# Performance work log

Measured on AMD Instinct MI355X. Metric: run time of the kernel, lower is better.

The kernel has to match this reference:

```python
import jax, jax.numpy as jnp
import numpy as np

GROUPS = 32
EPS = 1e-6


def group_norm(x, scale, bias):
    B, C, H, W = x.shape
    xg = x.reshape(B, GROUPS, C // GROUPS, H, W)
    mean = xg.mean(axis=(2, 3, 4), keepdims=True)
    var = xg.var(axis=(2, 3, 4), keepdims=True)
    xg = (xg - mean) * jax.lax.rsqrt(var + EPS)
    x = xg.reshape(B, C, H, W)
    return x * scale[None, :, None, None] + bias[None, :, None, None]


def conv1x1(x, w, b):
    # x: [B,C,H,W], w: [O,C], b: [O]
    return jnp.einsum('bchw,oc->bohw', x, w) + b[None, :, None, None]


def setup_inputs() -> dict:
    key = jax.random.key(0)
    ks = jax.random.split(key, 6)
    B, C, H, W = 8, 256, 64, 64
    s = 1.0 / np.sqrt(C)
    return {
        'x': jax.random.normal(ks[0], (B, C, H, W), dtype=jnp.float32),
        'gn_scale': jnp.ones((C,), dtype=jnp.float32),
        'gn_bias': jnp.zeros((C,), dtype=jnp.float32),
        'wq': jax.random.normal(ks[1], (C, C), dtype=jnp.float32) * s,
        'bq': jnp.zeros((C,), dtype=jnp.float32),
        'wk': jax.random.normal(ks[2], (C, C), dtype=jnp.float32) * s,
        'bk': jnp.zeros((C,), dtype=jnp.float32),
        'wv': jax.random.normal(ks[3], (C, C), dtype=jnp.float32) * s,
        'bv': jnp.zeros((C,), dtype=jnp.float32),
        'wo': jax.random.normal(ks[4], (C, C), dtype=jnp.float32) * s,
        'bo': jnp.zeros((C,), dtype=jnp.float32),
    }


def reference(x, gn_scale, gn_bias, wq, bq, wk, bk, wv, bv, wo, bo):
    skip = x
    h = group_norm(x, gn_scale, gn_bias)
    B, C, H, W = h.shape
    N = H * W
    q = conv1x1(h, wq, bq).reshape(B, C, N)  # [B,C,N]
    k = conv1x1(h, wk, bk).reshape(B, C, N)
    v = conv1x1(h, wv, bv).reshape(B, C, N)
    # scores[b,i,j] = sum_c q[b,c,i] k[b,c,j] / sqrt(C)
    scores = jnp.einsum('bci,bcj->bij', q, k) / jnp.sqrt(jnp.float32(C))
    a = jax.nn.softmax(scores, axis=2)  # softmax over keys j
    # z[b,c,i] = sum_j v[b,c,j] a[b,i,j]
    z = jnp.einsum('bcj,bij->bci', v, a).reshape(B, C, H, W)
    z = conv1x1(z, wo, bo)
    return skip + z
```

## Files before the change

kernel.cpp:

```cpp
#include <hip/hip_runtime.h>
#include <math.h>

typedef __bf16 bf16;
typedef __bf16 bf16x8 __attribute__((ext_vector_type(8)));
typedef __bf16 bf16x4 __attribute__((ext_vector_type(4)));
typedef float  f32x4  __attribute__((ext_vector_type(4)));
typedef float  f32x16 __attribute__((ext_vector_type(16)));
typedef unsigned int u32;
typedef unsigned char u8;
typedef u32 u32x2 __attribute__((ext_vector_type(2)));
typedef u32 u32x4 __attribute__((ext_vector_type(4)));
typedef int  i32x8 __attribute__((ext_vector_type(8)));

#define MFMA(a, b, c)   __builtin_amdgcn_mfma_f32_16x16x32_bf16((a), (b), (c), 0, 0, 0)
#define MFMAS(a, b, c)                                                           \
  __builtin_amdgcn_mfma_scale_f32_32x32x64_f8f6f4((a), (b), (c), 0, 0,           \
                                                  0, 0x7f7f7f7f, 0, 0x7f7f7f7f)

#define GLOAD_LDS16(g, l)                                                        \
  __builtin_amdgcn_global_load_lds(                                              \
      (const __attribute__((address_space(1))) void*)(g),                        \
      (__attribute__((address_space(3))) void*)(l), 16, 0, 0)

static constexpr int B_ = 8, C_ = 256, N_ = 4096;
static constexpr float QSCALE = 0.09016844005556021f;
static constexpr float PBIAS  = 2.0f;

static constexpr size_t HT_OFF = 0;
static constexpr size_t QT_OFF = 16777216;
static constexpr size_t KT_OFF = 25165824;
static constexpr size_t V_OFF  = 33554432;
static constexpr size_t WQ_OFF = 41943040;
static constexpr size_t WK_OFF = WQ_OFF + 131072;
static constexpr size_t WV_OFF = WK_OFF + 131072;
static constexpr size_t WO_OFF = WV_OFF + 131072;
static constexpr size_t ZN_OFF = WO_OFF + 131072;
static constexpr size_t LS_OFF = ZN_OFF + 33554432;
static constexpr size_t PART_ELEMS = (size_t)B_ * C_ * N_;

__global__ __launch_bounds__(256) void wconv_kernel(
    const float* __restrict__ wq, const float* __restrict__ wk,
    const float* __restrict__ wv, const float* __restrict__ wo,
    bf16* __restrict__ oq, bf16* __restrict__ ok, bf16* __restrict__ ov, bf16* __restrict__ oo) {
  int i = blockIdx.x * 256 + threadIdx.x;
  oq[i] = (bf16)wq[i];
  ok[i] = (bf16)wk[i];
  ov[i] = (bf16)wv[i];
  oo[i] = (bf16)wo[i];
}

__global__ __launch_bounds__(512) void gn_kernel(
    const float* __restrict__ x, const float* __restrict__ gsc, const float* __restrict__ gbi,
    bf16* __restrict__ hT) {
  int b = blockIdx.x >> 5, g = blockIdx.x & 31, c0 = g * 8;
  int t = threadIdx.x;
  const float* base = x + ((size_t)(b * C_ + c0)) * N_;
  __shared__ bf16 xl[32768];
  float s = 0.f, ss = 0.f;
  const f32x4* b4 = (const f32x4*)base;
#pragma unroll
  for (int p = 0; p < 16; p++) {
    int u = t + p * 512;
    f32x4 v = b4[u];
    s  += v[0] + v[1] + v[2] + v[3];
    ss += v[0] * v[0] + v[1] * v[1] + v[2] * v[2] + v[3] * v[3];
    bf16x4 xv;
#pragma unroll
    for (int e = 0; e < 4; e++) xv[e] = (bf16)v[e];
    *(bf16x4*)(xl + u * 4) = xv;
  }
#pragma unroll
  for (int off = 1; off < 64; off <<= 1) {
    s  += __shfl_xor(s, off);
    ss += __shfl_xor(ss, off);
  }
  __shared__ float red[16];
  if ((t & 63) == 0) { red[(t >> 6) * 2] = s; red[(t >> 6) * 2 + 1] = ss; }
  __syncthreads();
  s = 0.f; ss = 0.f;
#pragma unroll
  for (int r = 0; r < 8; r++) { s += red[r * 2]; ss += red[r * 2 + 1]; }
  float mean = s * (1.f / 32768.f);
  float var  = ss * (1.f / 32768.f) - mean * mean;
  float rstd = rsqrtf(var + 1e-6f);
  float aa[8], bb[8];
#pragma unroll
  for (int cc = 0; cc < 8; cc++) {
    aa[cc] = rstd * gsc[c0 + cc];
    bb[cc] = gbi[c0 + cc] - mean * aa[cc];
  }
#pragma unroll
  for (int ii = 0; ii < 8; ii++) {
    int i = t + ii * 512;
    bf16x8 o;
#pragma unroll
    for (int cc = 0; cc < 8; cc++) o[cc] = (bf16)((float)xl[cc * 4096 + i] * aa[cc] + bb[cc]);
    *(bf16x8*)(hT + ((size_t)(b * N_ + i)) * C_ + c0) = o;
  }
}

__global__ __launch_bounds__(256) void qkv_kernel(
    const bf16* __restrict__ hT,
    const bf16* __restrict__ wqb, const bf16* __restrict__ wkb, const bf16* __restrict__ wvb,
    const float* __restrict__ bq, const float* __restrict__ bk, const float* __restrict__ bv,
    u8* __restrict__ qT8, u8* __restrict__ kT8, u8* __restrict__ v8) {
  int b = blockIdx.x >> 6, i0 = (blockIdx.x & 63) << 6;
  int t = threadIdx.x, w = t >> 6, lane = t & 63, quad = lane >> 4, l15 = lane & 15;
  __shared__ bf16 hl[64 * 264];
#pragma unroll
  for (int p = 0; p < 8; p++) {
    int u = t + p * 256, r = u >> 5, c16 = u & 31;
    *(bf16x8*)(hl + r * 264 + c16 * 8) =
        *(const bf16x8*)(hT + ((size_t)(b * N_ + i0 + r)) * C_ + c16 * 8);
  }
  __syncthreads();
  int cw0 = w * 64;

  f32x4 aq[4][4], ak[4][4];
#pragma unroll
  for (int a = 0; a < 4; a++)
#pragma unroll
    for (int bb2 = 0; bb2 < 4; bb2++) { aq[a][bb2] = (f32x4){0.f,0.f,0.f,0.f}; ak[a][bb2] = (f32x4){0.f,0.f,0.f,0.f}; }
  for (int kc = 0; kc < 8; kc++) {
    bf16x8 hb[4];
#pragma unroll
    for (int it = 0; it < 4; it++)
      hb[it] = *(const bf16x8*)(hl + (it * 16 + l15) * 264 + kc * 32 + quad * 8);
#pragma unroll
    for (int ct = 0; ct < 4; ct++) {
      bf16x8 wqf = *(const bf16x8*)(wqb + ((size_t)(cw0 + ct * 16 + l15)) * C_ + kc * 32 + quad * 8);
      bf16x8 wkf = *(const bf16x8*)(wkb + ((size_t)(cw0 + ct * 16 + l15)) * C_ + kc * 32 + quad * 8);
#pragma unroll
      for (int it = 0; it < 4; it++) {
        aq[ct][it] = MFMA(wqf, hb[it], aq[ct][it]);
        ak[ct][it] = MFMA(wkf, hb[it], ak[ct][it]);
      }
    }
  }
#pragma unroll
  for (int ct = 0; ct < 4; ct++)
#pragma unroll
    for (int it = 0; it < 4; it++) {
      int c4 = cw0 + ct * 16 + quad * 4;
      int i  = i0 + it * 16 + l15;
      f32x4 bq4 = *(const f32x4*)(bq + c4);
      f32x4 bk4 = *(const f32x4*)(bk + c4);
      float qv[4], kv[4];
#pragma unroll
      for (int r = 0; r < 4; r++) {
        qv[r] = (aq[ct][it][r] + bq4[r]) * (QSCALE * 4.0f);
        kv[r] = (ak[ct][it][r] + bk4[r]) * 0.25f;
      }
      u32 qd = (u32)__builtin_amdgcn_cvt_pk_fp8_f32(qv[0], qv[1], 0, false);
      qd = (u32)__builtin_amdgcn_cvt_pk_fp8_f32(qv[2], qv[3], (int)qd, true);
      u32 kd = (u32)__builtin_amdgcn_cvt_pk_fp8_f32(kv[0], kv[1], 0, false);
      kd = (u32)__builtin_amdgcn_cvt_pk_fp8_f32(kv[2], kv[3], (int)kd, true);
      *(u32*)(qT8 + ((size_t)(b * N_ + i)) * C_ + c4) = qd;
      *(u32*)(kT8 + ((size_t)(b * N_ + i)) * C_ + c4) = kd;
    }

  f32x4 av[4][4];
#pragma unroll
  for (int a = 0; a < 4; a++)
#pragma unroll
    for (int bb2 = 0; bb2 < 4; bb2++) av[a][bb2] = (f32x4){0.f,0.f,0.f,0.f};
  for (int kc = 0; kc < 8; kc++) {
    bf16x8 ha[4];
#pragma unroll
    for (int it = 0; it < 4; it++)
      ha[it] = *(const bf16x8*)(hl + (it * 16 + l15) * 264 + kc * 32 + quad * 8);
#pragma unroll
    for (int ct = 0; ct < 4; ct++) {
      bf16x8 wvf = *(const bf16x8*)(wvb + ((size_t)(cw0 + ct * 16 + l15)) * C_ + kc * 32 + quad * 8);
#pragma unroll
      for (int it = 0; it < 4; it++) av[it][ct] = MFMA(ha[it], wvf, av[it][ct]);
    }
  }
#pragma unroll
  for (int it = 0; it < 4; it++)
#pragma unroll
    for (int ct = 0; ct < 4; ct++) {
      int c  = cw0 + ct * 16 + l15;
      int i4 = i0 + it * 16 + quad * 4;
      float bvc = bv[c];
      float vv4[4];
#pragma unroll
      for (int r = 0; r < 4; r++) vv4[r] = av[it][ct][r] + bvc;
      u32 vd = (u32)__builtin_amdgcn_cvt_pk_fp8_f32(vv4[0], vv4[1], 0, false);
      vd = (u32)__builtin_amdgcn_cvt_pk_fp8_f32(vv4[2], vv4[3], (int)vd, true);
      *(u32*)(v8 + ((size_t)(b * C_ + c)) * N_ + i4) = vd;
    }
}

__global__ __launch_bounds__(256, 2) void attn_kernel(
    const u8* __restrict__ qT8, const u8* __restrict__ kT8, const u8* __restrict__ v8,
    bf16* __restrict__ zNum, float* __restrict__ lsum) {
  int blk = blockIdx.x;
  int sp = blk >> 8;
  int b = blk & 7;
  int i0 = ((blk >> 3) & 31) << 7;
  int t = threadIdx.x, w = t >> 6, lane = t & 63;
  int r31 = lane & 31, h = lane >> 5;
  __shared__ __align__(16) u8 lds8[2 * 32768];

  int iw = i0 + w * 32;
  const u8* qrow = qT8 + ((size_t)(b * N_ + iw + r31)) * C_ + h * 32;
  i32x8 qB[4];
#pragma unroll
  for (int m = 0; m < 4; m++) qB[m] = *(const i32x8*)(qrow + m * 64);

  f32x16 of[8];
#pragma unroll
  for (int ct = 0; ct < 8; ct++)
#pragma unroll
    for (int e = 0; e < 16; e++) of[ct][e] = 0.f;
  float lacc = 0.f;

  int ks = r31 & 7;
  int kr_off = lane >> 4;
  int kc_pos = lane & 15;
  int vr_off = lane >> 2;
  int vc_pos = lane & 3;

  auto stage = [&](int jts, int buf) {
    int j0s = sp * 2048 + jts * 64;
    u8* kb = lds8 + buf * 32768;
    u8* vb = kb + 16384;
#pragma unroll
    for (int p = 0; p < 4; p++) {
      int idx = w * 4 + p;
      int r = idx * 4 + kr_off;
      int chunk = kc_pos ^ (r & 7);
      GLOAD_LDS16(kT8 + ((size_t)(b * N_ + j0s + r)) * C_ + chunk * 16, kb + idx * 1024);
    }
#pragma unroll
    for (int p = 0; p < 4; p++) {
      int idx = w * 4 + p;
      int c = idx * 16 + vr_off;
      int chunk = vc_pos ^ ((c >> 1) & 3);
      GLOAD_LDS16(v8 + ((size_t)(b * C_ + c)) * N_ + j0s + chunk * 16, vb + idx * 1024);
    }
  };

  stage(0, 0);

  for (int jt = 0; jt < 32; jt++) {
    int cur = jt & 1;
    __builtin_amdgcn_s_barrier();
    stage(jt < 31 ? jt + 1 : 31, cur ^ 1);
    asm volatile("s_waitcnt vmcnt(8)" ::: "memory");
    __builtin_amdgcn_s_barrier();
    const u8* kTl = lds8 + cur * 32768;
    const u8* vl  = kTl + 16384;

    u32 PG0[4], PG1[4];
#pragma unroll
    for (int g = 0; g < 2; g++) {
      f32x16 st;
#pragma unroll
      for (int e = 0; e < 16; e++) st[e] = -PBIAS;
      const u8* krow = kTl + (g * 32 + r31) * 256;
#pragma unroll
      for (int m = 0; m < 4; m++) {
        int cd = m * 4 + h * 2;
        union { i32x8 v; u32x4 h4[2]; } kf;
        kf.h4[0] = *(const u32x4*)(krow + ((cd ^ ks) * 16));
        kf.h4[1] = *(const u32x4*)(krow + (((cd + 1) ^ ks) * 16));
        st = MFMAS(kf.v, qB[m], st);
      }
#pragma unroll
      for (int b4 = 0; b4 < 4; b4++) {
        float p0 = __builtin_amdgcn_exp2f(st[b4 * 4 + 0]);
        float p1 = __builtin_amdgcn_exp2f(st[b4 * 4 + 1]);
        float p2 = __builtin_amdgcn_exp2f(st[b4 * 4 + 2]);
        float p3 = __builtin_amdgcn_exp2f(st[b4 * 4 + 3]);
        lacc += (p0 + p1) + (p2 + p3);
        u32 d = (u32)__builtin_amdgcn_cvt_pk_fp8_f32(p0, p1, 0, false);
        d = (u32)__builtin_amdgcn_cvt_pk_fp8_f32(p2, p3, (int)d, true);
        if (g == 0) PG0[b4] = d; else PG1[b4] = d;
      }
    }

    u32 A[8];
#pragma unroll
    for (int b4 = 0; b4 < 4; b4++) {
      u32x2 rr = __builtin_amdgcn_permlane32_swap(PG0[b4], PG1[b4], false, false);
      A[2 * b4]     = rr[0];
      A[2 * b4 + 1] = rr[1];
    }
    i32x8 pA;
#pragma unroll
    for (int e = 0; e < 8; e++) pA[e] = (int)A[e];

#pragma unroll
    for (int ct = 0; ct < 8; ct++) {
      int c = ct * 32 + r31;
      int vs = (c >> 1) & 3;
      const u8* vrow = vl + c * 64;
      union { i32x8 v; u32x4 h4[2]; } vB;
      vB.h4[0] = *(const u32x4*)(vrow + (((2 * h) ^ vs) * 16));
      vB.h4[1] = *(const u32x4*)(vrow + (((2 * h + 1) ^ vs) * 16));
      of[ct] = MFMAS(pA, vB.v, of[ct]);
    }
  }

  lacc += __shfl_xor(lacc, 32);
  if (h == 0)
    lsum[((size_t)(sp * 8 + b)) * N_ + iw + r31] = lacc;
  bf16* zn = zNum + (size_t)sp * PART_ELEMS;
#pragma unroll
  for (int ct = 0; ct < 8; ct++) {
    int c = ct * 32 + r31;
#pragma unroll
    for (int g = 0; g < 4; g++) {
      bf16x4 zv;
#pragma unroll
      for (int e = 0; e < 4; e++) zv[e] = (bf16)of[ct][g * 4 + e];
      int i4 = iw + 8 * g + 4 * h;
      *(bf16x4*)(zn + ((size_t)(b * C_ + c)) * N_ + i4) = zv;
    }
  }
}

__global__ __launch_bounds__(256) void combine_kernel(
    const bf16* __restrict__ zNum, const float* __restrict__ lsum,
    const bf16* __restrict__ wob, const float* __restrict__ bo,
    const float* __restrict__ x, float* __restrict__ out) {
  int b = blockIdx.x >> 6, i0 = (blockIdx.x & 63) << 6;
  int t = threadIdx.x, w = t >> 6, lane = t & 63, quad = lane >> 4, l15 = lane & 15;
  __shared__ bf16 zl[64 * 264];
  __shared__ float linv[64];

  if (t < 64) {
    size_t ii = (size_t)b * N_ + i0 + t;
    linv[t] = 1.f / (lsum[ii] + lsum[ii + (size_t)8 * N_]);
  }
  __syncthreads();

#pragma unroll
  for (int p = 0; p < 16; p++) {
    int u = t + p * 256, c = u >> 4, ii = (u & 15) * 4;
    size_t base = ((size_t)(b * C_ + c)) * N_ + i0 + ii;
    bf16x4 z0 = *(const bf16x4*)(zNum + base);
    bf16x4 z1 = *(const bf16x4*)(zNum + PART_ELEMS + base);
#pragma unroll
    for (int e = 0; e < 4; e++)
      zl[(ii + e) * 264 + c] = (bf16)(((float)z0[e] + (float)z1[e]) * linv[ii + e]);
  }
  __syncthreads();

  f32x4 oa[4][4];
#pragma unroll
  for (int a = 0; a < 4; a++)
#pragma unroll
    for (int bb2 = 0; bb2 < 4; bb2++) oa[a][bb2] = (f32x4){0.f, 0.f, 0.f, 0.f};
  for (int kc = 0; kc < 8; kc++) {
    bf16x8 za[4];
#pragma unroll
    for (int it = 0; it < 4; it++)
      za[it] = *(const bf16x8*)(zl + (it * 16 + l15) * 264 + kc * 32 + quad * 8);
#pragma unroll
    for (int ctl = 0; ctl < 4; ctl++) {
      bf16x8 wf = *(const bf16x8*)(wob + ((size_t)(w * 64 + ctl * 16 + l15)) * C_ + kc * 32 + quad * 8);
#pragma unroll
      for (int it = 0; it < 4; it++) oa[ctl][it] = MFMA(za[it], wf, oa[ctl][it]);
    }
  }
#pragma unroll
  for (int ctl = 0; ctl < 4; ctl++)
#pragma unroll
    for (int it = 0; it < 4; it++) {
      int c = w * 64 + ctl * 16 + l15;
      size_t base = ((size_t)(b * C_ + c)) * N_ + i0 + it * 16 + quad * 4;
      f32x4 xs = *(const f32x4*)(x + base);
      float boc = bo[c];
      f32x4 o4;
#pragma unroll
      for (int r = 0; r < 4; r++) o4[r] = oa[ctl][it][r] + boc + xs[r];
      *(f32x4*)(out + base) = o4;
    }
}

extern "C" void kernel_launch(void* const* d_in, const int* in_sizes, int n_in,
                              void* d_out, int out_size, void* d_ws, size_t ws_size,
                              hipStream_t stream) {
  const float* x   = (const float*)d_in[0];
  const float* gsc = (const float*)d_in[1];
  const float* gbi = (const float*)d_in[2];
  const float* wq  = (const float*)d_in[3];
  const float* bq  = (const float*)d_in[4];
  const float* wk  = (const float*)d_in[5];
  const float* bk  = (const float*)d_in[6];
  const float* wv  = (const float*)d_in[7];
  const float* bv  = (const float*)d_in[8];
  const float* wo  = (const float*)d_in[9];
  const float* bo  = (const float*)d_in[10];

  char* ws = (char*)d_ws;
  bf16* hT   = (bf16*)(ws + HT_OFF);
  u8*   qT8  = (u8*)(ws + QT_OFF);
  u8*   kT8  = (u8*)(ws + KT_OFF);
  u8*   v8   = (u8*)(ws + V_OFF);
  bf16* wqb  = (bf16*)(ws + WQ_OFF);
  bf16* wkb  = (bf16*)(ws + WK_OFF);
  bf16* wvb  = (bf16*)(ws + WV_OFF);
  bf16* wob  = (bf16*)(ws + WO_OFF);
  bf16* zNum = (bf16*)(ws + ZN_OFF);
  float* lsum = (float*)(ws + LS_OFF);

  wconv_kernel<<<256, 256, 0, stream>>>(wq, wk, wv, wo, wqb, wkb, wvb, wob);
  gn_kernel<<<256, 512, 0, stream>>>(x, gsc, gbi, hT);
  qkv_kernel<<<512, 256, 0, stream>>>(hT, wqb, wkb, wvb, bq, bk, bv, qT8, kT8, v8);
  attn_kernel<<<512, 256, 0, stream>>>(qT8, kT8, v8, zNum, lsum);
  combine_kernel<<<512, 256, 0, stream>>>(zNum, lsum, wob, bo, x, (float*)d_out);
}
```

Before: 251.8 us.

## Split attention keys four ways, shrink LDS to three buffers for higher occupancy

Templates the attention kernel on the number of key splits and launches 4 splits (1024 blocks) when the workspace is large enough, so more blocks are available to fill the CUs. LDS is cut from two K+V double buffers to two K buffers plus one V buffer, with an extra wait and barrier before the PV step, and launch bounds are raised to 3 blocks per CU. The hT region is reused for the first partial-output buffer, and the combine kernel sums SP partials. The cost is more partial-output traffic in the combine kernel and an extra barrier per key tile.

```diff
diff --git a/kernel.cpp b/kernel.cpp
--- a/kernel.cpp
+++ b/kernel.cpp
@@ -34,9 +34,12 @@
 static constexpr size_t WK_OFF = WQ_OFF + 131072;
 static constexpr size_t WV_OFF = WK_OFF + 131072;
 static constexpr size_t WO_OFF = WV_OFF + 131072;
-static constexpr size_t ZN_OFF = WO_OFF + 131072;
-static constexpr size_t LS_OFF = ZN_OFF + 33554432;
+static constexpr size_t LS_OFF = WO_OFF + 131072;
+static constexpr size_t ZN2_OFF = LS_OFF + 524288;
 static constexpr size_t PART_ELEMS = (size_t)B_ * C_ * N_;
+static constexpr size_t PART_BYTES = PART_ELEMS * 2;
+static constexpr size_t WS_NEED4 = ZN2_OFF + 3 * PART_BYTES;
+static constexpr size_t WS_NEED2 = ZN2_OFF + 1 * PART_BYTES;
 
 __global__ __launch_bounds__(256) void wconv_kernel(
     const float* __restrict__ wq, const float* __restrict__ wk,
@@ -192,16 +195,19 @@
     }
 }
 
-__global__ __launch_bounds__(256, 2) void attn_kernel(
+template <int SP>
+__global__ __launch_bounds__(256, 3) void attn_kernel(
     const u8* __restrict__ qT8, const u8* __restrict__ kT8, const u8* __restrict__ v8,
-    bf16* __restrict__ zNum, float* __restrict__ lsum) {
+    bf16* __restrict__ zn0, bf16* __restrict__ znR, float* __restrict__ lsum) {
+  constexpr int NKEY = N_ / SP;
+  constexpr int NJT  = NKEY / 64;
   int blk = blockIdx.x;
   int sp = blk >> 8;
   int b = blk & 7;
   int i0 = ((blk >> 3) & 31) << 7;
   int t = threadIdx.x, w = t >> 6, lane = t & 63;
   int r31 = lane & 31, h = lane >> 5;
-  __shared__ __align__(16) u8 lds8[2 * 32768];
+  __shared__ __align__(16) u8 lds8[3 * 16384];
 
   int iw = i0 + w * 32;
   const u8* qrow = qT8 + ((size_t)(b * N_ + iw + r31)) * C_ + h * 32;
@@ -221,11 +227,11 @@
   int kc_pos = lane & 15;
   int vr_off = lane >> 2;
   int vc_pos = lane & 3;
-
-  auto stage = [&](int jts, int buf) {
-    int j0s = sp * 2048 + jts * 64;
-    u8* kb = lds8 + buf * 32768;
-    u8* vb = kb + 16384;
+  int spBase = sp * NKEY;
+  u8* vb = lds8 + 32768;
+
+  auto stageK = [&](int jts, u8* kb) {
+    int j0s = spBase + jts * 64;
 #pragma unroll
     for (int p = 0; p < 4; p++) {
       int idx = w * 4 + p;
@@ -233,6 +239,9 @@
       int chunk = kc_pos ^ (r & 7);
       GLOAD_LDS16(kT8 + ((size_t)(b * N_ + j0s + r)) * C_ + chunk * 16, kb + idx * 1024);
     }
+  };
+  auto stageV = [&](int jts) {
+    int j0s = spBase + jts * 64;
 #pragma unroll
     for (int p = 0; p < 4; p++) {
       int idx = w * 4 + p;
@@ -242,16 +251,15 @@
     }
   };
 
-  stage(0, 0);
-
-  for (int jt = 0; jt < 32; jt++) {
-    int cur = jt & 1;
+  stageK(0, lds8);
+
+  for (int jt = 0; jt < NJT; jt++) {
     __builtin_amdgcn_s_barrier();
-    stage(jt < 31 ? jt + 1 : 31, cur ^ 1);
+    stageV(jt);
+    stageK(jt < NJT - 1 ? jt + 1 : jt, lds8 + (((jt + 1) & 1) << 14));
     asm volatile("s_waitcnt vmcnt(8)" ::: "memory");
     __builtin_amdgcn_s_barrier();
-    const u8* kTl = lds8 + cur * 32768;
-    const u8* vl  = kTl + 16384;
+    const u8* kTl = lds8 + ((jt & 1) << 14);
 
     u32 PG0[4], PG1[4];
 #pragma unroll
@@ -292,11 +300,14 @@
 #pragma unroll
     for (int e = 0; e < 8; e++) pA[e] = (int)A[e];
 
+    asm volatile("s_waitcnt vmcnt(4)" ::: "memory");
+    __builtin_amdgcn_s_barrier();
+
 #pragma unroll
     for (int ct = 0; ct < 8; ct++) {
       int c = ct * 32 + r31;
       int vs = (c >> 1) & 3;
-      const u8* vrow = vl + c * 64;
+      const u8* vrow = vb + c * 64;
       union { i32x8 v; u32x4 h4[2]; } vB;
       vB.h4[0] = *(const u32x4*)(vrow + (((2 * h) ^ vs) * 16));
       vB.h4[1] = *(const u32x4*)(vrow + (((2 * h + 1) ^ vs) * 16));
@@ -307,7 +318,7 @@
   lacc += __shfl_xor(lacc, 32);
   if (h == 0)
     lsum[((size_t)(sp * 8 + b)) * N_ + iw + r31] = lacc;
-  bf16* zn = zNum + (size_t)sp * PART_ELEMS;
+  bf16* zn = (sp == 0) ? zn0 : (znR + (size_t)(sp - 1) * PART_ELEMS);
 #pragma unroll
   for (int ct = 0; ct < 8; ct++) {
     int c = ct * 32 + r31;
@@ -322,8 +333,10 @@
   }
 }
 
+template <int SP>
 __global__ __launch_bounds__(256) void combine_kernel(
-    const bf16* __restrict__ zNum, const float* __restrict__ lsum,
+    const bf16* __restrict__ zn0, const bf16* __restrict__ znR,
+    const float* __restrict__ lsum,
     const bf16* __restrict__ wob, const float* __restrict__ bo,
     const float* __restrict__ x, float* __restrict__ out) {
   int b = blockIdx.x >> 6, i0 = (blockIdx.x & 63) << 6;
@@ -333,7 +346,10 @@
 
   if (t < 64) {
     size_t ii = (size_t)b * N_ + i0 + t;
-    linv[t] = 1.f / (lsum[ii] + lsum[ii + (size_t)8 * N_]);
+    float s = 0.f;
+#pragma unroll
+    for (int p = 0; p < SP; p++) s += lsum[(size_t)(p * 8) * N_ + ii];
+    linv[t] = 1.f / s;
   }
   __syncthreads();
 
@@ -341,11 +357,17 @@
   for (int p = 0; p < 16; p++) {
     int u = t + p * 256, c = u >> 4, ii = (u & 15) * 4;
     size_t base = ((size_t)(b * C_ + c)) * N_ + i0 + ii;
-    bf16x4 z0 = *(const bf16x4*)(zNum + base);
-    bf16x4 z1 = *(const bf16x4*)(zNum + PART_ELEMS + base);
+    float zsum[4] = {0.f, 0.f, 0.f, 0.f};
+#pragma unroll
+    for (int q = 0; q < SP; q++) {
+      const bf16* src = (q == 0) ? zn0 : (znR + (size_t)(q - 1) * PART_ELEMS);
+      bf16x4 z = *(const bf16x4*)(src + base);
+#pragma unroll
+      for (int e = 0; e < 4; e++) zsum[e] += (float)z[e];
+    }
 #pragma unroll
     for (int e = 0; e < 4; e++)
-      zl[(ii + e) * 264 + c] = (bf16)(((float)z0[e] + (float)z1[e]) * linv[ii + e]);
+      zl[(ii + e) * 264 + c] = (bf16)(zsum[e] * linv[ii + e]);
   }
   __syncthreads();
 
@@ -405,12 +427,18 @@
   bf16* wkb  = (bf16*)(ws + WK_OFF);
   bf16* wvb  = (bf16*)(ws + WV_OFF);
   bf16* wob  = (bf16*)(ws + WO_OFF);
-  bf16* zNum = (bf16*)(ws + ZN_OFF);
   float* lsum = (float*)(ws + LS_OFF);
+  bf16* zn0  = (bf16*)(ws + HT_OFF);
+  bf16* znR  = (bf16*)(ws + ZN2_OFF);
 
   wconv_kernel<<<256, 256, 0, stream>>>(wq, wk, wv, wo, wqb, wkb, wvb, wob);
   gn_kernel<<<256, 512, 0, stream>>>(x, gsc, gbi, hT);
   qkv_kernel<<<512, 256, 0, stream>>>(hT, wqb, wkb, wvb, bq, bk, bv, qT8, kT8, v8);
-  attn_kernel<<<512, 256, 0, stream>>>(qT8, kT8, v8, zNum, lsum);
-  combine_kernel<<<512, 256, 0, stream>>>(zNum, lsum, wob, bo, x, (float*)d_out);
-}
+  if (ws_size >= WS_NEED4) {
+    attn_kernel<4><<<1024, 256, 0, stream>>>(qT8, kT8, v8, zn0, znR, lsum);
+    combine_kernel<4><<<512, 256, 0, stream>>>(zn0, znR, lsum, wob, bo, x, (float*)d_out);
+  } else {
+    attn_kernel<2><<<512, 256, 0, stream>>>(qT8, kT8, v8, zn0, znR, lsum);
+    combine_kernel<2><<<512, 256, 0, stream>>>(zn0, znR, lsum, wob, bo, x, (float*)d_out);
+  }
+}
```

After: 630.1 us. +150.3%, slower.
